# Performance work log

Measured on AMD Instinct MI355X. Metric: run time of the kernel, lower is better.

The kernel has to match this reference:

```python
import jax, jax.numpy as jnp
import numpy as np
import math

NB_FEATURES = 256

def _softmax_kernel(x, projection_matrix):
    # x: [B,H,N,D], projection_matrix: [D,F] -> [B,H,N,F]
    x_proj = jnp.einsum('bhnd,df->bhnf', x, projection_matrix)
    x_proj = x_proj - jnp.max(x_proj, axis=-1, keepdims=True)
    return jnp.exp(x_proj) / math.sqrt(projection_matrix.shape[-1])

def setup_inputs() -> dict:
    key = jax.random.key(0)
    k1, k2, k3, k4 = jax.random.split(key, 4)
    B, H, N, D = 2, 16, 4096, 64
    q = jax.random.normal(k1, (B, H, N, D), dtype=jnp.float32)
    k = jax.random.normal(k2, (B, H, N, D), dtype=jnp.float32)
    v = jax.random.normal(k3, (B, H, N, D), dtype=jnp.float32)
    projection_matrix = jax.random.normal(k4, (D, NB_FEATURES), dtype=jnp.float32)
    return {"q": q, "k": k, "v": v, "projection_matrix": projection_matrix}

def reference(q, k, v, projection_matrix):
    q_prime = _softmax_kernel(q, projection_matrix)  # [B,H,N,F]
    k_prime = _softmax_kernel(k, projection_matrix)  # [B,H,N,F]
    kv = jnp.einsum('bhnf,bhne->bhfe', k_prime, v)   # [B,H,F,E]
    denom = jnp.einsum('bhnf,bhf->bhn', q_prime, jnp.sum(k_prime, axis=-2) + 1e-06)
    z = 1.0 / denom[..., None]                        # [B,H,N,1]
    out = jnp.einsum('bhnf,bhfe->bhne', q_prime, kv)  # [B,H,N,E]
    return out * z
```

## Files before the change

### kernel.cpp

```cpp
#include <hip/hip_runtime.h>
#include <math.h>

typedef float f4 __attribute__((ext_vector_type(4)));
typedef float f32x4 __attribute__((ext_vector_type(4)));
typedef _Float16 h4 __attribute__((ext_vector_type(4)));
typedef _Float16 h8 __attribute__((ext_vector_type(8)));

#define BH 32
#define NN 4096
#define DD 64
#define FF 256
#define EE 64
#define SPLITS 8
#define ROWS_K 512
#define QB 8
#define ROWS_Q 512
#define ST 72
#define SK 136
#define STF 264

#define MFMA(a, b, c) __builtin_amdgcn_mfma_f32_16x16x32_f16((a), (b), (c), 0, 0, 0)

__device__ inline h8 cvt2(f4 x0, f4 x1) {
  h8 r;
  r[0] = (_Float16)x0.x; r[1] = (_Float16)x0.y;
  r[2] = (_Float16)x0.z; r[3] = (_Float16)x0.w;
  r[4] = (_Float16)x1.x; r[5] = (_Float16)x1.y;
  r[6] = (_Float16)x1.z; r[7] = (_Float16)x1.w;
  return r;
}

__global__ __launch_bounds__(512, 2) void fa_kside(
    const float* __restrict__ kin, const float* __restrict__ vin,
    const float* __restrict__ P, float* __restrict__ kv_part,
    float* __restrict__ ksum_part) {
  __shared__ _Float16 Pt[FF * ST];
  __shared__ _Float16 kpt[FF * SK];
  __shared__ _Float16 vt[EE * SK];
  __shared__ float ks_lds[8 * FF];

  const int t = threadIdx.x;
  const int w = t >> 6, lane = t & 63;
  const int g = lane >> 4, fl = lane & 15;
  const int bh = blockIdx.x >> 3, split = blockIdx.x & 7;
  const int bhs = blockIdx.x;
  const int k0 = g * 8;

  {
    const f4* Pg4 = (const f4*)P;
#pragma unroll
    for (int i = 0; i < 8; ++i) {
      int idx = t + i * 512;
      f4 pv = Pg4[idx];
      int d = idx >> 6, f0 = (idx & 63) * 4;
      Pt[(f0 + 0) * ST + d] = (_Float16)pv.x;
      Pt[(f0 + 1) * ST + d] = (_Float16)pv.y;
      Pt[(f0 + 2) * ST + d] = (_Float16)pv.z;
      Pt[(f0 + 3) * ST + d] = (_Float16)pv.w;
    }
  }

  f32x4 kvacc[2][4];
#pragma unroll
  for (int mi = 0; mi < 2; ++mi)
#pragma unroll
    for (int nt = 0; nt < 4; ++nt) kvacc[mi][nt] = (f32x4){0.f, 0.f, 0.f, 0.f};
  float ksum_acc[16];
#pragma unroll
  for (int T = 0; T < 16; ++T) ksum_acc[T] = 0.f;

  const size_t base = (size_t)bh * NN * DD + (size_t)split * ROWS_K * DD;
  __syncthreads();

  for (int tile = 0; tile < 4; ++tile) {
    if (tile) __syncthreads();
    const int r0g = tile * 128 + w * 16;

    const float* krow = kin + base + (size_t)(r0g + fl) * DD;
    h8 a0 = cvt2(*(const f4*)&krow[k0], *(const f4*)&krow[k0 + 4]);
    h8 a1 = cvt2(*(const f4*)&krow[32 + k0], *(const f4*)&krow[32 + k0 + 4]);

    {
      const float* vb = vin + base + (size_t)r0g * DD + lane;
      h8 tv0, tv1;
#pragma unroll
      for (int j = 0; j < 8; ++j) tv0[j] = (_Float16)vb[j * DD];
#pragma unroll
      for (int j = 0; j < 8; ++j) tv1[j] = (_Float16)vb[(8 + j) * DD];
      *(h8*)&vt[lane * SK + w * 16] = tv0;
      *(h8*)&vt[lane * SK + w * 16 + 8] = tv1;
    }

    f32x4 lac[16];
#pragma unroll
    for (int T = 0; T < 16; ++T) {
      int ncol = T * 16 + fl;
      h8 b0 = *(const h8*)&Pt[ncol * ST + k0];
      h8 b1 = *(const h8*)&Pt[ncol * ST + 32 + k0];
      f32x4 c = {0.f, 0.f, 0.f, 0.f};
      c = MFMA(a0, b0, c);
      c = MFMA(a1, b1, c);
      lac[T] = c;
    }

    float mrow[4];
#pragma unroll
    for (int rg = 0; rg < 4; ++rg) {
      float m = lac[0][rg];
#pragma unroll
      for (int T = 1; T < 16; ++T) m = fmaxf(m, lac[T][rg]);
#pragma unroll
      for (int off = 1; off <= 8; off <<= 1)
        m = fmaxf(m, __shfl_xor(m, off, 64));
      mrow[rg] = m;
    }

#pragma unroll
    for (int T = 0; T < 16; ++T) {
      int ncol = T * 16 + fl;
      h4 kp;
#pragma unroll
      for (int rg = 0; rg < 4; ++rg) {
        float ev = __expf(lac[T][rg] - mrow[rg]) * 0.0625f;
        _Float16 hv = (_Float16)ev;
        ksum_acc[T] += (float)hv;
        kp[rg] = hv;
      }
      *(h4*)&kpt[ncol * SK + w * 16 + g * 4] = kp;
    }
    __syncthreads();

#pragma unroll
    for (int kst = 0; kst < 4; ++kst) {
      h8 vbf[4];
#pragma unroll
      for (int nt = 0; nt < 4; ++nt)
        vbf[nt] = *(const h8*)&vt[(nt * 16 + fl) * SK + kst * 32 + k0];
#pragma unroll
      for (int mi = 0; mi < 2; ++mi) {
        h8 ka = *(const h8*)&kpt[((2 * w + mi) * 16 + fl) * SK + kst * 32 + k0];
#pragma unroll
        for (int nt = 0; nt < 4; ++nt)
          kvacc[mi][nt] = MFMA(ka, vbf[nt], kvacc[mi][nt]);
      }
    }
  }

  float* kvp = kv_part + (size_t)bhs * (FF * EE);
#pragma unroll
  for (int mi = 0; mi < 2; ++mi)
#pragma unroll
    for (int nt = 0; nt < 4; ++nt)
#pragma unroll
      for (int rg = 0; rg < 4; ++rg) {
        int f = (2 * w + mi) * 16 + g * 4 + rg;
        int e = nt * 16 + fl;
        kvp[f * EE + e] = kvacc[mi][nt][rg];
      }

#pragma unroll
  for (int T = 0; T < 16; ++T) {
    float s = ksum_acc[T];
    s += __shfl_xor(s, 16, 64);
    s += __shfl_xor(s, 32, 64);
    if (lane < 16) ks_lds[w * FF + T * 16 + lane] = s;
  }
  __syncthreads();
  if (t < FF) {
    float s = 0.f;
#pragma unroll
    for (int wi = 0; wi < 8; ++wi) s += ks_lds[wi * FF + t];
    ksum_part[(size_t)bhs * FF + t] = s;
  }
}

__global__ __launch_bounds__(256) void fa_reduce(
    const float* __restrict__ kv_part, const float* __restrict__ ksum_part,
    _Float16* __restrict__ kvt_g, float* __restrict__ ksum_g) {
  __shared__ _Float16 tl[EE * 18];
  const int b = blockIdx.x, t = threadIdx.x;
  if (b < 512) {
    const int bh = b >> 4, c = b & 15;
#pragma unroll
    for (int i = 0; i < 4; ++i) {
      int idx = i * 256 + t;
      int fr = idx >> 6, e = idx & 63;
      float s = 0.f;
#pragma unroll
      for (int sp = 0; sp < SPLITS; ++sp)
        s += kv_part[(size_t)(bh * SPLITS + sp) * (FF * EE) + (c * 16 + fr) * EE + e];
      tl[e * 18 + fr] = (_Float16)s;
    }
    __syncthreads();
    unsigned int* og = (unsigned int*)kvt_g + (size_t)bh * 8192;
#pragma unroll
    for (int i = 0; i < 2; ++i) {
      int idx = i * 256 + t;
      int e = idx >> 3, fp = (idx & 7) * 2;
      og[e * 128 + c * 8 + (idx & 7)] = *(unsigned int*)&tl[e * 18 + fp];
    }
  } else {
    const int bh = b - 512;
    float s = 0.f;
#pragma unroll
    for (int sp = 0; sp < SPLITS; ++sp)
      s += ksum_part[(size_t)(bh * SPLITS + sp) * FF + t];
    ksum_g[bh * FF + t] = s + 1e-6f;
  }
}

__global__ __launch_bounds__(512, 2) void fa_qside(
    const float* __restrict__ qin, const float* __restrict__ P,
    const _Float16* __restrict__ kvt_g, const float* __restrict__ ksum_g,
    float* __restrict__ out) {
  __shared__ _Float16 Pt[FF * ST];
  __shared__ _Float16 kvt[EE * STF];
  __shared__ _Float16 qpt[8 * 16 * STF];

  const int t = threadIdx.x;
  const int w = t >> 6, lane = t & 63;
  const int g = lane >> 4, fl = lane & 15;
  const int bh = blockIdx.x >> 3, qb = blockIdx.x & 7;
  const int k0 = g * 8;

  {
    const f4* Pg4 = (const f4*)P;
#pragma unroll
    for (int i = 0; i < 8; ++i) {
      int idx = t + i * 512;
      f4 pv = Pg4[idx];
      int d = idx >> 6, f0 = (idx & 63) * 4;
      Pt[(f0 + 0) * ST + d] = (_Float16)pv.x;
      Pt[(f0 + 1) * ST + d] = (_Float16)pv.y;
      Pt[(f0 + 2) * ST + d] = (_Float16)pv.z;
      Pt[(f0 + 3) * ST + d] = (_Float16)pv.w;
    }
  }
  {
    const h8* src = (const h8*)(kvt_g + (size_t)bh * FF * EE);
#pragma unroll
    for (int i = 0; i < 4; ++i) {
      int idx = t + i * 512;
      int e = idx >> 5, f0 = (idx & 31) * 8;
      *(h8*)&kvt[e * STF + f0] = src[idx];
    }
  }
  float ksr[16];
#pragma unroll
  for (int T = 0; T < 16; ++T) ksr[T] = ksum_g[bh * FF + T * 16 + fl];
  __syncthreads();

  _Float16* myqpt = qpt + w * 16 * STF;
  const size_t base = (size_t)bh * NN * DD + (size_t)qb * ROWS_Q * DD;
  float* ob = out + (size_t)bh * NN * EE + (size_t)qb * ROWS_Q * EE;

  for (int st = 0; st < 4; ++st) {
    const int r0g = st * 128 + w * 16;
    const float* qrow = qin + base + (size_t)(r0g + fl) * DD;
    h8 a0 = cvt2(*(const f4*)&qrow[k0], *(const f4*)&qrow[k0 + 4]);
    h8 a1 = cvt2(*(const f4*)&qrow[32 + k0], *(const f4*)&qrow[32 + k0 + 4]);

    f32x4 lac[16];
#pragma unroll
    for (int T = 0; T < 16; ++T) {
      int ncol = T * 16 + fl;
      h8 b0 = *(const h8*)&Pt[ncol * ST + k0];
      h8 b1 = *(const h8*)&Pt[ncol * ST + 32 + k0];
      f32x4 c = {0.f, 0.f, 0.f, 0.f};
      c = MFMA(a0, b0, c);
      c = MFMA(a1, b1, c);
      lac[T] = c;
    }

    float mrow[4];
#pragma unroll
    for (int rg = 0; rg < 4; ++rg) {
      float m = lac[0][rg];
#pragma unroll
      for (int T = 1; T < 16; ++T) m = fmaxf(m, lac[T][rg]);
#pragma unroll
      for (int off = 1; off <= 8; off <<= 1)
        m = fmaxf(m, __shfl_xor(m, off, 64));
      mrow[rg] = m;
    }

    float den[4] = {0.f, 0.f, 0.f, 0.f};
#pragma unroll
    for (int T = 0; T < 16; ++T) {
      int ncol = T * 16 + fl;
#pragma unroll
      for (int rg = 0; rg < 4; ++rg) {
        float ev = __expf(lac[T][rg] - mrow[rg]) * 0.0625f;
        _Float16 hv = (_Float16)ev;
        den[rg] += (float)hv * ksr[T];
        myqpt[(g * 4 + rg) * STF + ncol] = hv;
      }
    }
#pragma unroll
    for (int rg = 0; rg < 4; ++rg) {
#pragma unroll
      for (int off = 1; off <= 8; off <<= 1)
        den[rg] += __shfl_xor(den[rg], off, 64);
    }

    f32x4 oacc[4];
#pragma unroll
    for (int nt = 0; nt < 4; ++nt) oacc[nt] = (f32x4){0.f, 0.f, 0.f, 0.f};
#pragma unroll
    for (int kst = 0; kst < 8; ++kst) {
      h8 aq = *(const h8*)&myqpt[fl * STF + kst * 32 + k0];
#pragma unroll
      for (int nt = 0; nt < 4; ++nt) {
        h8 bq = *(const h8*)&kvt[(nt * 16 + fl) * STF + kst * 32 + k0];
        oacc[nt] = MFMA(aq, bq, oacc[nt]);
      }
    }

    float* obt = ob + (size_t)r0g * EE;
#pragma unroll
    for (int rg = 0; rg < 4; ++rg) {
      float inv = 1.0f / den[rg];
#pragma unroll
      for (int nt = 0; nt < 4; ++nt) {
        int e = nt * 16 + fl;
        obt[(g * 4 + rg) * EE + e] = oacc[nt][rg] * inv;
      }
    }
  }
}

extern "C" void kernel_launch(void* const* d_in, const int* in_sizes, int n_in,
                              void* d_out, int out_size, void* d_ws,
                              size_t ws_size, hipStream_t stream) {
  (void)in_sizes;
  (void)n_in;
  (void)out_size;
  (void)ws_size;
  const float* q = (const float*)d_in[0];
  const float* k = (const float*)d_in[1];
  const float* v = (const float*)d_in[2];
  const float* P = (const float*)d_in[3];
  float* out = (float*)d_out;

  float* kv_part = (float*)d_ws;
  float* ksum_part = kv_part + 256 * 16384;
  _Float16* kvt_g = (_Float16*)(ksum_part + 256 * 256);
  float* ksum_g = (float*)(kvt_g + 32 * 16384);

  hipLaunchKernelGGL(fa_kside, dim3(BH * SPLITS), dim3(512), 0, stream, k, v, P,
                     kv_part, ksum_part);
  hipLaunchKernelGGL(fa_reduce, dim3(544), dim3(256), 0, stream, kv_part,
                     ksum_part, kvt_g, ksum_g);
  hipLaunchKernelGGL(fa_qside, dim3(BH * QB), dim3(512), 0, stream, q, P, kvt_g,
                     ksum_g, out);
}
```

Before: 176.0 us.

## Precompute fp16 projection, swizzle LDS, double splits and fuse ksum into MFMA

```diff
diff --git a/kernel.cpp b/kernel.cpp
--- a/kernel.cpp
+++ b/kernel.cpp
@@ -11,13 +11,10 @@
 #define DD 64
 #define FF 256
 #define EE 64
-#define SPLITS 8
-#define ROWS_K 512
-#define QB 8
-#define ROWS_Q 512
-#define ST 72
-#define SK 136
-#define STF 264
+#define SPLITS 16
+#define ROWS_K 256
+#define QB 16
+#define ROWS_Q 256
 
 #define MFMA(a, b, c) __builtin_amdgcn_mfma_f32_16x16x32_f16((a), (b), (c), 0, 0, 0)
 
@@ -30,55 +27,48 @@
   return r;
 }
 
-__global__ __launch_bounds__(512, 2) void fa_kside(
+__global__ __launch_bounds__(512) void fa_prep(const float* __restrict__ P,
+                                               _Float16* __restrict__ PT) {
+  const int e = blockIdx.x * 512 + threadIdx.x;
+  const int f = e & 255, dq = e >> 8;
+  h4 o;
+#pragma unroll
+  for (int j = 0; j < 4; ++j) o[j] = (_Float16)P[(dq * 4 + j) * FF + f];
+  *(h4*)&PT[f * DD + dq * 4] = o;
+}
+
+__global__ __launch_bounds__(512, 4) void fa_kside(
     const float* __restrict__ kin, const float* __restrict__ vin,
-    const float* __restrict__ P, float* __restrict__ kv_part,
+    const _Float16* __restrict__ PT, float* __restrict__ kv_part,
     float* __restrict__ ksum_part) {
-  __shared__ _Float16 Pt[FF * ST];
-  __shared__ _Float16 kpt[FF * SK];
-  __shared__ _Float16 vt[EE * SK];
-  __shared__ float ks_lds[8 * FF];
+  __shared__ _Float16 kpt[FF * 128];
+  __shared__ _Float16 vt[EE * 128];
 
   const int t = threadIdx.x;
   const int w = t >> 6, lane = t & 63;
   const int g = lane >> 4, fl = lane & 15;
-  const int bh = blockIdx.x >> 3, split = blockIdx.x & 7;
+  const int bh = blockIdx.x >> 4, split = blockIdx.x & 15;
   const int bhs = blockIdx.x;
   const int k0 = g * 8;
-
-  {
-    const f4* Pg4 = (const f4*)P;
-#pragma unroll
-    for (int i = 0; i < 8; ++i) {
-      int idx = t + i * 512;
-      f4 pv = Pg4[idx];
-      int d = idx >> 6, f0 = (idx & 63) * 4;
-      Pt[(f0 + 0) * ST + d] = (_Float16)pv.x;
-      Pt[(f0 + 1) * ST + d] = (_Float16)pv.y;
-      Pt[(f0 + 2) * ST + d] = (_Float16)pv.z;
-      Pt[(f0 + 3) * ST + d] = (_Float16)pv.w;
-    }
-  }
+  const int key = fl & 7;
 
   f32x4 kvacc[2][4];
 #pragma unroll
   for (int mi = 0; mi < 2; ++mi)
 #pragma unroll
     for (int nt = 0; nt < 4; ++nt) kvacc[mi][nt] = (f32x4){0.f, 0.f, 0.f, 0.f};
-  float ksum_acc[16];
-#pragma unroll
-  for (int T = 0; T < 16; ++T) ksum_acc[T] = 0.f;
+  f32x4 ksacc[2];
+  ksacc[0] = (f32x4){0.f, 0.f, 0.f, 0.f};
+  ksacc[1] = (f32x4){0.f, 0.f, 0.f, 0.f};
+  h8 ones;
+#pragma unroll
+  for (int j = 0; j < 8; ++j) ones[j] = (_Float16)1.0f;
 
   const size_t base = (size_t)bh * NN * DD + (size_t)split * ROWS_K * DD;
-  __syncthreads();
-
-  for (int tile = 0; tile < 4; ++tile) {
+
+  for (int tile = 0; tile < 2; ++tile) {
     if (tile) __syncthreads();
     const int r0g = tile * 128 + w * 16;
-
-    const float* krow = kin + base + (size_t)(r0g + fl) * DD;
-    h8 a0 = cvt2(*(const f4*)&krow[k0], *(const f4*)&krow[k0 + 4]);
-    h8 a1 = cvt2(*(const f4*)&krow[32 + k0], *(const f4*)&krow[32 + k0 + 4]);
 
     {
       const float* vb = vin + base + (size_t)r0g * DD + lane;
@@ -87,16 +77,20 @@
       for (int j = 0; j < 8; ++j) tv0[j] = (_Float16)vb[j * DD];
 #pragma unroll
       for (int j = 0; j < 8; ++j) tv1[j] = (_Float16)vb[(8 + j) * DD];
-      *(h8*)&vt[lane * SK + w * 16] = tv0;
-      *(h8*)&vt[lane * SK + w * 16 + 8] = tv1;
-    }
+      *(h8*)&vt[lane * 128 + (((w * 2 + 0) ^ (lane & 7)) << 3)] = tv0;
+      *(h8*)&vt[lane * 128 + (((w * 2 + 1) ^ (lane & 7)) << 3)] = tv1;
+    }
+
+    const float* krow = kin + base + (size_t)(r0g + fl) * DD;
+    h8 a0 = cvt2(*(const f4*)&krow[k0], *(const f4*)&krow[k0 + 4]);
+    h8 a1 = cvt2(*(const f4*)&krow[32 + k0], *(const f4*)&krow[36 + k0]);
 
     f32x4 lac[16];
 #pragma unroll
     for (int T = 0; T < 16; ++T) {
-      int ncol = T * 16 + fl;
-      h8 b0 = *(const h8*)&Pt[ncol * ST + k0];
-      h8 b1 = *(const h8*)&Pt[ncol * ST + 32 + k0];
+      const int ncol = T * 16 + fl;
+      h8 b0 = *(const h8*)&PT[ncol * DD + k0];
+      h8 b1 = *(const h8*)&PT[ncol * DD + 32 + k0];
       f32x4 c = {0.f, 0.f, 0.f, 0.f};
       c = MFMA(a0, b0, c);
       c = MFMA(a1, b1, c);
@@ -117,16 +111,13 @@
 
 #pragma unroll
     for (int T = 0; T < 16; ++T) {
-      int ncol = T * 16 + fl;
+      const int ncol = T * 16 + fl;
       h4 kp;
 #pragma unroll
-      for (int rg = 0; rg < 4; ++rg) {
-        float ev = __expf(lac[T][rg] - mrow[rg]) * 0.0625f;
-        _Float16 hv = (_Float16)ev;
-        ksum_acc[T] += (float)hv;
-        kp[rg] = hv;
-      }
-      *(h4*)&kpt[ncol * SK + w * 16 + g * 4] = kp;
+      for (int rg = 0; rg < 4; ++rg)
+        kp[rg] = (_Float16)(__expf(lac[T][rg] - mrow[rg]) * 0.0625f);
+      *(h4*)&kpt[ncol * 128 + (((w * 2 + (g >> 1)) ^ key) << 3) + (g & 1) * 4] =
+          kp;
     }
     __syncthreads();
 
@@ -135,13 +126,16 @@
       h8 vbf[4];
 #pragma unroll
       for (int nt = 0; nt < 4; ++nt)
-        vbf[nt] = *(const h8*)&vt[(nt * 16 + fl) * SK + kst * 32 + k0];
+        vbf[nt] =
+            *(const h8*)&vt[(nt * 16 + fl) * 128 + (((kst * 4 + g) ^ key) << 3)];
 #pragma unroll
       for (int mi = 0; mi < 2; ++mi) {
-        h8 ka = *(const h8*)&kpt[((2 * w + mi) * 16 + fl) * SK + kst * 32 + k0];
+        h8 ka = *(const h8*)&kpt[((2 * w + mi) * 16 + fl) * 128 +
+                                 (((kst * 4 + g) ^ key) << 3)];
 #pragma unroll
         for (int nt = 0; nt < 4; ++nt)
           kvacc[mi][nt] = MFMA(ka, vbf[nt], kvacc[mi][nt]);
+        ksacc[mi] = MFMA(ka, ones, ksacc[mi]);
       }
     }
   }
@@ -152,25 +146,16 @@
 #pragma unroll
     for (int nt = 0; nt < 4; ++nt)
 #pragma unroll
-      for (int rg = 0; rg < 4; ++rg) {
-        int f = (2 * w + mi) * 16 + g * 4 + rg;
-        int e = nt * 16 + fl;
-        kvp[f * EE + e] = kvacc[mi][nt][rg];
-      }
-
-#pragma unroll
-  for (int T = 0; T < 16; ++T) {
-    float s = ksum_acc[T];
-    s += __shfl_xor(s, 16, 64);
-    s += __shfl_xor(s, 32, 64);
-    if (lane < 16) ks_lds[w * FF + T * 16 + lane] = s;
-  }
-  __syncthreads();
-  if (t < FF) {
-    float s = 0.f;
-#pragma unroll
-    for (int wi = 0; wi < 8; ++wi) s += ks_lds[wi * FF + t];
-    ksum_part[(size_t)bhs * FF + t] = s;
+      for (int rg = 0; rg < 4; ++rg)
+        kvp[((2 * w + mi) * 16 + g * 4 + rg) * EE + nt * 16 + fl] =
+            kvacc[mi][nt][rg];
+  if (fl == 0) {
+#pragma unroll
+    for (int mi = 0; mi < 2; ++mi)
+#pragma unroll
+      for (int rg = 0; rg < 4; ++rg)
+        ksum_part[(size_t)bhs * FF + (2 * w + mi) * 16 + g * 4 + rg] =
+            ksacc[mi][rg];
   }
 }
 
@@ -188,7 +173,8 @@
       float s = 0.f;
 #pragma unroll
       for (int sp = 0; sp < SPLITS; ++sp)
-        s += kv_part[(size_t)(bh * SPLITS + sp) * (FF * EE) + (c * 16 + fr) * EE + e];
+        s += kv_part[(size_t)(bh * SPLITS + sp) * (FF * EE) +
+                     (c * 16 + fr) * EE + e];
       tl[e * 18 + fr] = (_Float16)s;
     }
     __syncthreads();
@@ -196,8 +182,8 @@
 #pragma unroll
     for (int i = 0; i < 2; ++i) {
       int idx = i * 256 + t;
-      int e = idx >> 3, fp = (idx & 7) * 2;
-      og[e * 128 + c * 8 + (idx & 7)] = *(unsigned int*)&tl[e * 18 + fp];
+      int e = idx >> 3, j = idx & 7;
+      og[e * 128 + c * 8 + j] = *(unsigned int*)&tl[e * 18 + j * 2];
     }
   } else {
     const int bh = b - 512;
@@ -209,31 +195,28 @@
   }
 }
 
-__global__ __launch_bounds__(512, 2) void fa_qside(
-    const float* __restrict__ qin, const float* __restrict__ P,
+__global__ __launch_bounds__(512, 4) void fa_qside(
+    const float* __restrict__ qin, const _Float16* __restrict__ PTg,
     const _Float16* __restrict__ kvt_g, const float* __restrict__ ksum_g,
     float* __restrict__ out) {
-  __shared__ _Float16 Pt[FF * ST];
-  __shared__ _Float16 kvt[EE * STF];
-  __shared__ _Float16 qpt[8 * 16 * STF];
+  __shared__ _Float16 PTl[FF * DD];
+  __shared__ _Float16 kvt[EE * FF];
+  __shared__ _Float16 qpt[8 * 16 * 64];
 
   const int t = threadIdx.x;
   const int w = t >> 6, lane = t & 63;
   const int g = lane >> 4, fl = lane & 15;
-  const int bh = blockIdx.x >> 3, qb = blockIdx.x & 7;
+  const int bh = blockIdx.x >> 4, qb = blockIdx.x & 15;
   const int k0 = g * 8;
+  const int key = fl & 7;
 
   {
-    const f4* Pg4 = (const f4*)P;
-#pragma unroll
-    for (int i = 0; i < 8; ++i) {
+    const h8* src = (const h8*)PTg;
+#pragma unroll
+    for (int i = 0; i < 4; ++i) {
       int idx = t + i * 512;
-      f4 pv = Pg4[idx];
-      int d = idx >> 6, f0 = (idx & 63) * 4;
-      Pt[(f0 + 0) * ST + d] = (_Float16)pv.x;
-      Pt[(f0 + 1) * ST + d] = (_Float16)pv.y;
-      Pt[(f0 + 2) * ST + d] = (_Float16)pv.z;
-      Pt[(f0 + 3) * ST + d] = (_Float16)pv.w;
+      int f = idx >> 3, c0 = idx & 7;
+      *(h8*)&PTl[f * DD + ((c0 ^ (f & 7)) << 3)] = src[idx];
     }
   }
   {
@@ -241,31 +224,29 @@
 #pragma unroll
     for (int i = 0; i < 4; ++i) {
       int idx = t + i * 512;
-      int e = idx >> 5, f0 = (idx & 31) * 8;
-      *(h8*)&kvt[e * STF + f0] = src[idx];
-    }
-  }
-  float ksr[16];
-#pragma unroll
-  for (int T = 0; T < 16; ++T) ksr[T] = ksum_g[bh * FF + T * 16 + fl];
+      int e = idx >> 5, c0 = idx & 31;
+      *(h8*)&kvt[e * FF + ((c0 ^ (e & 7)) << 3)] = src[idx];
+    }
+  }
   __syncthreads();
 
-  _Float16* myqpt = qpt + w * 16 * STF;
+  _Float16* myqpt = qpt + w * 1024;
+  const float* ksb = ksum_g + bh * FF;
   const size_t base = (size_t)bh * NN * DD + (size_t)qb * ROWS_Q * DD;
   float* ob = out + (size_t)bh * NN * EE + (size_t)qb * ROWS_Q * EE;
 
-  for (int st = 0; st < 4; ++st) {
+  for (int st = 0; st < 2; ++st) {
     const int r0g = st * 128 + w * 16;
     const float* qrow = qin + base + (size_t)(r0g + fl) * DD;
     h8 a0 = cvt2(*(const f4*)&qrow[k0], *(const f4*)&qrow[k0 + 4]);
-    h8 a1 = cvt2(*(const f4*)&qrow[32 + k0], *(const f4*)&qrow[32 + k0 + 4]);
+    h8 a1 = cvt2(*(const f4*)&qrow[32 + k0], *(const f4*)&qrow[36 + k0]);
 
     f32x4 lac[16];
 #pragma unroll
     for (int T = 0; T < 16; ++T) {
-      int ncol = T * 16 + fl;
-      h8 b0 = *(const h8*)&Pt[ncol * ST + k0];
-      h8 b1 = *(const h8*)&Pt[ncol * ST + 32 + k0];
+      const int ncol = T * 16 + fl;
+      h8 b0 = *(const h8*)&PTl[ncol * DD + (((0 * 4 + g) ^ key) << 3)];
+      h8 b1 = *(const h8*)&PTl[ncol * DD + (((1 * 4 + g) ^ key) << 3)];
       f32x4 c = {0.f, 0.f, 0.f, 0.f};
       c = MFMA(a0, b0, c);
       c = MFMA(a1, b1, c);
@@ -285,17 +266,39 @@
     }
 
     float den[4] = {0.f, 0.f, 0.f, 0.f};
-#pragma unroll
-    for (int T = 0; T < 16; ++T) {
-      int ncol = T * 16 + fl;
-#pragma unroll
-      for (int rg = 0; rg < 4; ++rg) {
-        float ev = __expf(lac[T][rg] - mrow[rg]) * 0.0625f;
-        _Float16 hv = (_Float16)ev;
-        den[rg] += (float)hv * ksr[T];
-        myqpt[(g * 4 + rg) * STF + ncol] = hv;
+    f32x4 oacc[4];
+#pragma unroll
+    for (int nt = 0; nt < 4; ++nt) oacc[nt] = (f32x4){0.f, 0.f, 0.f, 0.f};
+
+#pragma unroll
+    for (int p = 0; p < 4; ++p) {
+#pragma unroll
+      for (int tt = 0; tt < 4; ++tt) {
+        const int T = p * 4 + tt;
+        const float ks = ksb[T * 16 + fl];
+#pragma unroll
+        for (int rg = 0; rg < 4; ++rg) {
+          float ev = __expf(lac[T][rg] - mrow[rg]) * 0.0625f;
+          _Float16 hv = (_Float16)ev;
+          den[rg] += (float)hv * ks;
+          const int r = g * 4 + rg;
+          myqpt[r * 64 + (((tt * 2 + (fl >> 3)) ^ (r & 7)) << 3) + (fl & 7)] =
+              hv;
+        }
       }
-    }
+#pragma unroll
+      for (int k2 = 0; k2 < 2; ++k2) {
+        const int kst = p * 2 + k2;
+        h8 aq = *(const h8*)&myqpt[fl * 64 + (((k2 * 4 + g) ^ key) << 3)];
+#pragma unroll
+        for (int nt = 0; nt < 4; ++nt) {
+          h8 bq = *(const h8*)&kvt[(nt * 16 + fl) * FF +
+                                   (((kst * 4 + g) ^ key) << 3)];
+          oacc[nt] = MFMA(aq, bq, oacc[nt]);
+        }
+      }
+    }
+
 #pragma unroll
     for (int rg = 0; rg < 4; ++rg) {
 #pragma unroll
@@ -303,28 +306,13 @@
         den[rg] += __shfl_xor(den[rg], off, 64);
     }
 
-    f32x4 oacc[4];
-#pragma unroll
-    for (int nt = 0; nt < 4; ++nt) oacc[nt] = (f32x4){0.f, 0.f, 0.f, 0.f};
-#pragma unroll
-    for (int kst = 0; kst < 8; ++kst) {
-      h8 aq = *(const h8*)&myqpt[fl * STF + kst * 32 + k0];
-#pragma unroll
-      for (int nt = 0; nt < 4; ++nt) {
-        h8 bq = *(const h8*)&kvt[(nt * 16 + fl) * STF + kst * 32 + k0];
-        oacc[nt] = MFMA(aq, bq, oacc[nt]);
-      }
-    }
-
     float* obt = ob + (size_t)r0g * EE;
 #pragma unroll
     for (int rg = 0; rg < 4; ++rg) {
       float inv = 1.0f / den[rg];
 #pragma unroll
-      for (int nt = 0; nt < 4; ++nt) {
-        int e = nt * 16 + fl;
-        obt[(g * 4 + rg) * EE + e] = oacc[nt][rg] * inv;
-      }
+      for (int nt = 0; nt < 4; ++nt)
+        obt[(g * 4 + rg) * EE + nt * 16 + fl] = oacc[nt][rg] * inv;
     }
   }
 }
@@ -343,14 +331,16 @@
   float* out = (float*)d_out;
 
   float* kv_part = (float*)d_ws;
-  float* ksum_part = kv_part + 256 * 16384;
-  _Float16* kvt_g = (_Float16*)(ksum_part + 256 * 256);
-  float* ksum_g = (float*)(kvt_g + 32 * 16384);
-
-  hipLaunchKernelGGL(fa_kside, dim3(BH * SPLITS), dim3(512), 0, stream, k, v, P,
-                     kv_part, ksum_part);
+  float* ksum_part = kv_part + (size_t)512 * 16384;
+  _Float16* kvt_g = (_Float16*)(ksum_part + 512 * 256);
+  float* ksum_g = (float*)(kvt_g + (size_t)BH * FF * EE);
+  _Float16* PT = (_Float16*)(ksum_g + BH * FF);
+
+  hipLaunchKernelGGL(fa_prep, dim3(8), dim3(512), 0, stream, P, PT);
+  hipLaunchKernelGGL(fa_kside, dim3(BH * SPLITS), dim3(512), 0, stream, k, v,
+                     PT, kv_part, ksum_part);
   hipLaunchKernelGGL(fa_reduce, dim3(544), dim3(256), 0, stream, kv_part,
                      ksum_part, kvt_g, ksum_g);
-  hipLaunchKernelGGL(fa_qside, dim3(BH * QB), dim3(512), 0, stream, q, P, kvt_g,
-                     ksum_g, out);
-}
+  hipLaunchKernelGGL(fa_qside, dim3(BH * QB), dim3(512), 0, stream, q, PT,
+                     kvt_g, ksum_g, out);
+}
```

Result: slower. 300.9 us (+71.0%).
